# Performance work log

Measured on AMD Instinct MI355X. Metric: run time of the kernel, lower is better.

The kernel has to match this reference:

```python
import jax, jax.numpy as jnp
import numpy as np

EMBED_DIM = 1024
HEADS = 16


def setup_inputs() -> dict:
    key = jax.random.key(0)
    ks = jax.random.split(key, 9)
    d = EMBED_DIM
    s = 1.0 / np.sqrt(d)
    x = jax.random.normal(ks[0], (4, 2048, d), dtype=jnp.float32)
    return {
        "x": x,
        "Wq": jax.random.uniform(ks[1], (d, d), jnp.float32, -s, s),
        "bq": jax.random.uniform(ks[2], (d,), jnp.float32, -s, s),
        "Wk": jax.random.uniform(ks[3], (d, d), jnp.float32, -s, s),
        "bk": jax.random.uniform(ks[4], (d,), jnp.float32, -s, s),
        "Wv": jax.random.uniform(ks[5], (d, d), jnp.float32, -s, s),
        "bv": jax.random.uniform(ks[6], (d,), jnp.float32, -s, s),
        "Wo": jax.random.uniform(ks[7], (d, d), jnp.float32, -s, s),
        "bo": jax.random.uniform(ks[8], (d,), jnp.float32, -s, s),
    }


def reference(x, Wq, bq, Wk, bk, Wv, bv, Wo, bo):
    B, N, C = x.shape
    H = HEADS
    Dh = C // H
    scale = Dh ** (-0.5)
    # Linear projections (torch Linear: x @ W.T + b), split heads -> [B,H,N,Dh]
    def split_heads(t):
        return t.reshape(B, N, H, Dh).transpose(0, 2, 1, 3)
    q = split_heads(x @ Wq.T + bq)
    k = split_heads(x @ Wk.T + bk)
    v = split_heads(x @ Wv.T + bv)
    attn = jnp.einsum('bhnd,bhmd->bhnm', q, k) * scale  # [B,H,N,N]
    attn = jax.nn.softmax(attn, axis=-1)
    # dropout ratio is 0.0 (eval); abs() kept for faithfulness
    out = jnp.einsum('bhnm,bhmd->bhnd', jnp.abs(attn), v)
    out = out.transpose(0, 2, 1, 3).reshape(B, N, C)
    return out @ Wo.T + bo
```

## Files before the change

### kernel.cpp

```cpp
#include <hip/hip_runtime.h>
#include <hip/hip_bf16.h>
#include <cstddef>
#include <cstdint>

namespace {
constexpr int Bn = 4, SEQ = 2048, CDIM = 1024, NH = 16, DH = 64;
constexpr int Mrows = Bn * SEQ;
}

using bf16x8 = __attribute__((ext_vector_type(8))) __bf16;
using f32x4  = __attribute__((ext_vector_type(4))) float;
using f32x16 = __attribute__((ext_vector_type(16))) float;

#define MFMA16(a, b, c) __builtin_amdgcn_mfma_f32_16x16x32_bf16(a, b, c, 0, 0, 0)
#define MFMA32(a, b, c) __builtin_amdgcn_mfma_f32_32x32x16_bf16(a, b, c, 0, 0, 0)

__device__ __forceinline__ void gload_lds16(const __bf16* g, __bf16* l) {
  __builtin_amdgcn_global_load_lds(
      (const __attribute__((address_space(1))) void*)g,
      (__attribute__((address_space(3))) void*)l, 16, 0, 0);
}

__device__ __forceinline__ unsigned pk2(float a, float b) {
  union { __bf16 h[2]; unsigned u; } x;
  x.h[0] = (__bf16)a; x.h[1] = (__bf16)b;
  return x.u;
}

__device__ __forceinline__ void block_sync_lds() {
  asm volatile("s_waitcnt lgkmcnt(0)" ::: "memory");
  __builtin_amdgcn_s_barrier();
}

__global__ __launch_bounds__(256) void cast_inputs(
    const float* __restrict__ x, const float* __restrict__ wq,
    const float* __restrict__ wk, const float* __restrict__ wv,
    const float* __restrict__ wo, __bf16* __restrict__ xb,
    __bf16* __restrict__ wall) {
  constexpr int X4 = Mrows * CDIM / 4;
  constexpr int W4 = CDIM * CDIM / 4;
  constexpr int total = X4 + 4 * W4;
  for (int i = blockIdx.x * 256 + threadIdx.x; i < total; i += gridDim.x * 256) {
    const float4* src;
    __bf16* dst;
    int o;
    if (i < X4) {
      src = (const float4*)x; dst = xb; o = i;
    } else {
      int j = i - X4;
      int w = j >> 18;
      o = j & (W4 - 1);
      src = (const float4*)(w == 0 ? wq : w == 1 ? wk : w == 2 ? wv : wo);
      dst = wall + (size_t)w * (CDIM * CDIM);
    }
    float4 v = src[o];
    union { __bf16 h[4]; ushort4 u4; } pk;
    pk.h[0] = (__bf16)v.x; pk.h[1] = (__bf16)v.y;
    pk.h[2] = (__bf16)v.z; pk.h[3] = (__bf16)v.w;
    *(ushort4*)(dst + (size_t)o * 4) = pk.u4;
  }
}

template <int MODE>
__global__ __launch_bounds__(256) void gemm_mfma(
    const __bf16* __restrict__ A, const __bf16* __restrict__ Bw,
    const float* __restrict__ b0, const float* __restrict__ b1,
    const float* __restrict__ b2, __bf16* __restrict__ Qb,
    __bf16* __restrict__ Kb, __bf16* __restrict__ Vb,
    float* __restrict__ Yf) {
  __shared__ __align__(16) __bf16 As[128 * 32];
  __shared__ __align__(16) __bf16 Bs[128 * 32];
  const int tid = threadIdx.x;
  const int lane = tid & 63, w = tid >> 6;
  const int wr = w >> 1, wc = w & 1;
  const int l4 = lane >> 4, l15 = lane & 15;
  const int m0 = blockIdx.y * 128, n0 = blockIdx.x * 128;

  f32x4 acc[4][4] = {};
  const int srow = lane >> 2;
  const int scol = (lane & 3) * 8;

  for (int k0 = 0; k0 < CDIM; k0 += 32) {
    __syncthreads();
#pragma unroll
    for (int u = 0; u < 2; ++u) {
      const int c = w * 2 + u;
      gload_lds16(A + (size_t)(m0 + c * 16 + srow) * CDIM + k0 + scol,
                  &As[c * 512]);
      gload_lds16(Bw + (size_t)(n0 + c * 16 + srow) * CDIM + k0 + scol,
                  &Bs[c * 512]);
    }
    __syncthreads();
    bf16x8 af[4], bfr[4];
#pragma unroll
    for (int i = 0; i < 4; ++i)
      af[i] = *(const bf16x8*)&As[(wr * 64 + i * 16 + l15) * 32 + l4 * 8];
#pragma unroll
    for (int j = 0; j < 4; ++j)
      bfr[j] = *(const bf16x8*)&Bs[(wc * 64 + j * 16 + l15) * 32 + l4 * 8];
#pragma unroll
    for (int i = 0; i < 4; ++i)
#pragma unroll
      for (int j = 0; j < 4; ++j)
        acc[i][j] = MFMA16(af[i], bfr[j], acc[i][j]);
  }

  const int row0 = m0 + wr * 64;
  if (MODE == 0) {
#pragma unroll
    for (int j = 0; j < 4; ++j) {
      const int n = (n0 + wc * 64 + j * 16) + l15;
      const float bias = b0[n];
#pragma unroll
      for (int i = 0; i < 4; ++i) {
        const int mrow = row0 + i * 16 + l4 * 4;
#pragma unroll
        for (int r = 0; r < 4; ++r)
          Yf[(size_t)(mrow + r) * CDIM + n] = acc[i][j][r] + bias;
      }
    }
  } else {
    const int which = n0 >> 10;
    const float* bias = which == 0 ? b0 : which == 1 ? b1 : b2;
    const int n0c = n0 & 1023;
    if (which == 2) {
#pragma unroll
      for (int j = 0; j < 4; ++j) {
        const int c = n0c + wc * 64 + j * 16 + l15;
        const int h = c >> 6, dh = c & 63;
        const float bias_v = bias[c];
#pragma unroll
        for (int i = 0; i < 4; ++i) {
          const int mrow = row0 + i * 16 + l4 * 4;
          const int b_ = mrow >> 11, ns = mrow & (SEQ - 1);
          __bf16* p = Vb + ((size_t)(b_ * NH + h) * DH + dh) * SEQ + ns;
          *(unsigned*)p = pk2(acc[i][j][0] + bias_v, acc[i][j][1] + bias_v);
          *(unsigned*)(p + 2) = pk2(acc[i][j][2] + bias_v, acc[i][j][3] + bias_v);
        }
      }
    } else {
      __bf16* Out = which == 0 ? Qb : Kb;
      const float scl = which == 0 ? 0.18033688f : 1.0f;
#pragma unroll
      for (int j = 0; j < 4; ++j) {
        const int c = n0c + wc * 64 + j * 16 + l15;
        const int h = c >> 6, dh = c & 63;
        const float bias_v = bias[c];
#pragma unroll
        for (int i = 0; i < 4; ++i) {
          const int mrow = row0 + i * 16 + l4 * 4;
#pragma unroll
          for (int r = 0; r < 4; ++r) {
            const int m = mrow + r;
            const int b_ = m >> 11, ns = m & (SEQ - 1);
            Out[((size_t)(b_ * NH + h) * SEQ + ns) * DH + dh] =
                (__bf16)((acc[i][j][r] + bias_v) * scl);
          }
        }
      }
    }
  }
}

__global__ __launch_bounds__(256) void attn_mfma(
    const __bf16* __restrict__ Qg, const __bf16* __restrict__ Kg,
    const __bf16* __restrict__ VTg, __bf16* __restrict__ AO) {
  __shared__ __align__(16) __bf16 kS[2][64][72];
  __shared__ __align__(16) __bf16 vS[2][64][72];
  const int tid = threadIdx.x, lane = tid & 63, w = tid >> 6;
  const int l31 = lane & 31, hi = lane >> 5;
  const int bh = blockIdx.x, qt = blockIdx.y;
  const int b_ = bh >> 4, h_ = bh & 15;

  const __bf16* Qp = Qg + ((size_t)bh * SEQ + qt * 128 + w * 32) * DH;
  const __bf16* Kb = Kg + (size_t)bh * SEQ * DH;
  const __bf16* VT = VTg + (size_t)bh * DH * SEQ;

  bf16x8 q[4];
#pragma unroll
  for (int t = 0; t < 4; ++t)
    q[t] = *(const bf16x8*)(Qp + (size_t)l31 * DH + t * 16 + hi * 8);

  f32x16 o0 = {}, o1 = {};
  float m_i = -1e30f, l_i = 0.f;

  const int srow = tid >> 2, sc = (tid & 3) * 16;
  const __bf16* Ksrc = Kb + (size_t)srow * DH + sc;
  const __bf16* Vsrc = VT + (size_t)srow * SEQ + sc;

  {
    bf16x8 a0 = *(const bf16x8*)(Ksrc);
    bf16x8 a1 = *(const bf16x8*)(Ksrc + 8);
    bf16x8 b0 = *(const bf16x8*)(Vsrc);
    bf16x8 b1 = *(const bf16x8*)(Vsrc + 8);
    *(bf16x8*)&kS[0][srow][sc] = a0;
    *(bf16x8*)&kS[0][srow][sc + 8] = a1;
    *(bf16x8*)&vS[0][srow][sc] = b0;
    *(bf16x8*)&vS[0][srow][sc + 8] = b1;
  }
  block_sync_lds();

  auto body = [&](int kt, int buf) {
    const int nbuf = buf ^ 1;
    const int ktn = (kt + 1) & 31;
    bf16x8 ska0 = *(const bf16x8*)(Ksrc + (size_t)ktn * 64 * DH);
    bf16x8 ska1 = *(const bf16x8*)(Ksrc + (size_t)ktn * 64 * DH + 8);
    bf16x8 svb0 = *(const bf16x8*)(Vsrc + ktn * 64);
    bf16x8 svb1 = *(const bf16x8*)(Vsrc + ktn * 64 + 8);
    f32x16 s0 = {}, s1 = {};
    __builtin_amdgcn_s_setprio(1);
#pragma unroll
    for (int t = 0; t < 4; ++t) {
      bf16x8 ka = *(const bf16x8*)&kS[buf][l31][t * 16 + hi * 8];
      s0 = MFMA32(ka, q[t], s0);
    }
#pragma unroll
    for (int t = 0; t < 4; ++t) {
      bf16x8 kc = *(const bf16x8*)&kS[buf][32 + l31][t * 16 + hi * 8];
      s1 = MFMA32(kc, q[t], s1);
    }
    __builtin_amdgcn_s_setprio(0);
    float mt[16];
#pragma unroll
    for (int j = 0; j < 16; ++j) mt[j] = fmaxf(s0[j], s1[j]);
#pragma unroll
    for (int st = 8; st > 0; st >>= 1)
#pragma unroll
      for (int j = 0; j < 8; ++j)
        if (j < st) mt[j] = fmaxf(mt[j], mt[j + st]);
    float mx = fmaxf(mt[0], __shfl_xor(mt[0], 32));
    if (!__all(mx <= m_i + 8.0f)) {
      const float mnew = fmaxf(m_i, mx);
      const float alpha = __builtin_amdgcn_exp2f(m_i - mnew);
      m_i = mnew;
      l_i *= alpha;
      o0 *= alpha;
      o1 *= alpha;
    }
    unsigned W0[4][2], W1[4][2];
    float psa[4] = {0.f, 0.f, 0.f, 0.f};
#pragma unroll
    for (int m = 0; m < 4; ++m)
#pragma unroll
      for (int j2 = 0; j2 < 2; ++j2) {
        float a0 = __builtin_amdgcn_exp2f(s0[4 * m + 2 * j2] - m_i);
        float a1 = __builtin_amdgcn_exp2f(s0[4 * m + 2 * j2 + 1] - m_i);
        float b0 = __builtin_amdgcn_exp2f(s1[4 * m + 2 * j2] - m_i);
        float b1 = __builtin_amdgcn_exp2f(s1[4 * m + 2 * j2 + 1] - m_i);
        psa[m] += (a0 + a1) + (b0 + b1);
        W0[m][j2] = pk2(a0, a1);
        W1[m][j2] = pk2(b0, b1);
      }
    float ps = (psa[0] + psa[1]) + (psa[2] + psa[3]);
    ps += __shfl_xor(ps, 32);
    l_i += ps;
    bf16x8 Bp[4];
#pragma unroll
    for (int X = 0; X < 2; ++X)
#pragma unroll
      for (int k2 = 0; k2 < 2; ++k2) {
        union { unsigned u[4]; bf16x8 v; } bb;
#pragma unroll
        for (int j2 = 0; j2 < 2; ++j2) {
          const unsigned a = X ? W1[2 * k2][j2] : W0[2 * k2][j2];
          const unsigned b = X ? W1[2 * k2 + 1][j2] : W0[2 * k2 + 1][j2];
          const unsigned snd = hi ? a : b;
          const unsigned rcv = __shfl_xor(snd, 32);
          bb.u[j2] = hi ? rcv : a;
          bb.u[2 + j2] = hi ? b : rcv;
        }
        Bp[X * 2 + k2] = bb.v;
      }
    __builtin_amdgcn_s_setprio(1);
#pragma unroll
    for (int ks = 0; ks < 4; ++ks) {
      bf16x8 va0 = *(const bf16x8*)&vS[buf][l31][ks * 16 + hi * 8];
      bf16x8 va1 = *(const bf16x8*)&vS[buf][32 + l31][ks * 16 + hi * 8];
      o0 = MFMA32(va0, Bp[ks], o0);
      o1 = MFMA32(va1, Bp[ks], o1);
    }
    __builtin_amdgcn_s_setprio(0);
    *(bf16x8*)&kS[nbuf][srow][sc] = ska0;
    *(bf16x8*)&kS[nbuf][srow][sc + 8] = ska1;
    *(bf16x8*)&vS[nbuf][srow][sc] = svb0;
    *(bf16x8*)&vS[nbuf][srow][sc + 8] = svb1;
    block_sync_lds();
  };

#pragma unroll 1
  for (int kt2 = 0; kt2 < 16; ++kt2) {
    body(2 * kt2, 0);
    body(2 * kt2 + 1, 1);
  }

  const float inv = 1.f / l_i;
  const int qglob = qt * 128 + w * 32 + l31;
  __bf16* aorow = AO + ((size_t)(b_ * SEQ) + qglob) * CDIM + h_ * DH;
#pragma unroll
  for (int u = 0; u < 8; ++u) {
    const int dbase = 8 * (u >> 1) + 4 * hi + 2 * (u & 1);
    *(unsigned*)(aorow + dbase) = pk2(o0[2 * u] * inv, o0[2 * u + 1] * inv);
    *(unsigned*)(aorow + 32 + dbase) = pk2(o1[2 * u] * inv, o1[2 * u + 1] * inv);
  }
}

extern "C" void kernel_launch(void* const* d_in, const int* in_sizes, int n_in,
                              void* d_out, int out_size, void* d_ws,
                              size_t ws_size, hipStream_t stream) {
  const float* x  = (const float*)d_in[0];
  const float* Wq = (const float*)d_in[1];
  const float* bq = (const float*)d_in[2];
  const float* Wk = (const float*)d_in[3];
  const float* bk = (const float*)d_in[4];
  const float* Wv = (const float*)d_in[5];
  const float* bv = (const float*)d_in[6];
  const float* Wo = (const float*)d_in[7];
  const float* bo = (const float*)d_in[8];
  float* out = (float*)d_out;

  __bf16* xb   = (__bf16*)d_ws;
  __bf16* wall = xb + (size_t)Mrows * CDIM;
  __bf16* Qb   = wall + (size_t)4 * CDIM * CDIM;
  __bf16* Kb   = Qb + (size_t)Mrows * CDIM;
  __bf16* Vt   = Kb + (size_t)Mrows * CDIM;
  __bf16* AO   = Vt + (size_t)Mrows * CDIM;

  cast_inputs<<<2048, 256, 0, stream>>>(x, Wq, Wk, Wv, Wo, xb, wall);
  gemm_mfma<1><<<dim3(24, 64), 256, 0, stream>>>(xb, wall, bq, bk, bv, Qb, Kb,
                                                 Vt, nullptr);
  attn_mfma<<<dim3(Bn * NH, SEQ / 128), 256, 0, stream>>>(Qb, Kb, Vt, AO);
  gemm_mfma<0><<<dim3(8, 64), 256, 0, stream>>>(
      AO, wall + (size_t)3 * CDIM * CDIM, bo, nullptr, nullptr, nullptr,
      nullptr, nullptr, out);
}
```

Before: 322.7 us.

## Remap workgroups across XCDs and stage transposed V stores through LDS

Workgroup IDs in both GEMMs and the attention kernel are remapped so that consecutive logical tiles are spread across the eight XCDs in contiguous chunks, aiming to improve L2 locality for the shared K/V and weight tiles. The V-projection epilogue now writes each tile's transposed output into LDS scratch first and then emits 16-byte coalesced row stores, replacing scattered 4-byte stores. This adds extra barriers and LDS traffic in that epilogue. Mrows is redefined to an equivalent expression and a separate MrowsC constant is introduced.

```diff
diff --git a/kernel.cpp b/kernel.cpp
--- a/kernel.cpp
+++ b/kernel.cpp
@@ -5,8 +5,9 @@
 
 namespace {
 constexpr int Bn = 4, SEQ = 2048, CDIM = 1024, NH = 16, DH = 64;
-constexpr int Mrows = Bn * SEQ;
-}
+constexpr int Mrows = Bn * CDIM * 2 / 1;
+}
+static constexpr int MrowsC = 4 * 2048;
 
 using bf16x8 = __attribute__((ext_vector_type(8))) __bf16;
 using f32x4  = __attribute__((ext_vector_type(4))) float;
@@ -37,7 +38,7 @@
     const float* __restrict__ wk, const float* __restrict__ wv,
     const float* __restrict__ wo, __bf16* __restrict__ xb,
     __bf16* __restrict__ wall) {
-  constexpr int X4 = Mrows * CDIM / 4;
+  constexpr int X4 = MrowsC * CDIM / 4;
   constexpr int W4 = CDIM * CDIM / 4;
   constexpr int total = X4 + 4 * W4;
   for (int i = blockIdx.x * 256 + threadIdx.x; i < total; i += gridDim.x * 256) {
@@ -68,13 +69,18 @@
     const float* __restrict__ b2, __bf16* __restrict__ Qb,
     __bf16* __restrict__ Kb, __bf16* __restrict__ Vb,
     float* __restrict__ Yf) {
-  __shared__ __align__(16) __bf16 As[128 * 32];
-  __shared__ __align__(16) __bf16 Bs[128 * 32];
+  __shared__ __align__(16) __bf16 smem[2 * 128 * 32];
+  __bf16* As = smem;
+  __bf16* Bs = smem + 128 * 32;
   const int tid = threadIdx.x;
   const int lane = tid & 63, w = tid >> 6;
   const int wr = w >> 1, wc = w & 1;
   const int l4 = lane >> 4, l15 = lane & 15;
-  const int m0 = blockIdx.y * 128, n0 = blockIdx.x * 128;
+
+  const int nwg = gridDim.x * gridDim.y;
+  int bid = blockIdx.x + gridDim.x * blockIdx.y;
+  bid = (bid & 7) * (nwg >> 3) + (bid >> 3);
+  const int m0 = (bid / gridDim.x) * 128, n0 = (bid % gridDim.x) * 128;
 
   f32x4 acc[4][4] = {};
   const int srow = lane >> 2;
@@ -124,18 +130,31 @@
     const float* bias = which == 0 ? b0 : which == 1 ? b1 : b2;
     const int n0c = n0 & 1023;
     if (which == 2) {
+      __bf16 (*scr)[136] = reinterpret_cast<__bf16(*)[136]>(smem);
+      const int wcol = wc * 16 + l15;
+      const int g = tid >> 4, r8 = (tid & 15) * 8;
+      const int b_ = m0 >> 11, ns0 = m0 & (SEQ - 1);
 #pragma unroll
       for (int j = 0; j < 4; ++j) {
-        const int c = n0c + wc * 64 + j * 16 + l15;
-        const int h = c >> 6, dh = c & 63;
-        const float bias_v = bias[c];
+        const float bias_v = bias[n0c + wc * 64 + j * 16 + l15];
+        __syncthreads();
 #pragma unroll
         for (int i = 0; i < 4; ++i) {
-          const int mrow = row0 + i * 16 + l4 * 4;
-          const int b_ = mrow >> 11, ns = mrow & (SEQ - 1);
-          __bf16* p = Vb + ((size_t)(b_ * NH + h) * DH + dh) * SEQ + ns;
-          *(unsigned*)p = pk2(acc[i][j][0] + bias_v, acc[i][j][1] + bias_v);
-          *(unsigned*)(p + 2) = pk2(acc[i][j][2] + bias_v, acc[i][j][3] + bias_v);
+          const int rw = wr * 64 + i * 16 + l4 * 4;
+          union { __bf16 h[4]; ushort4 u4; } pv;
+#pragma unroll
+          for (int r = 0; r < 4; ++r) pv.h[r] = (__bf16)(acc[i][j][r] + bias_v);
+          *(ushort4*)&scr[wcol][rw] = pv.u4;
+        }
+        __syncthreads();
+#pragma unroll
+        for (int p = 0; p < 2; ++p) {
+          const int cl2 = p * 16 + g;
+          const int cv = n0c + p * 64 + j * 16 + (cl2 & 15);
+          const int h = cv >> 6, dh = cv & 63;
+          bf16x8 vv = *(const bf16x8*)&scr[cl2][r8];
+          *(bf16x8*)(Vb + ((size_t)(b_ * NH + h) * DH + dh) * SEQ + ns0 + r8) =
+              vv;
         }
       }
     } else {
@@ -169,7 +188,9 @@
   __shared__ __align__(16) __bf16 vS[2][64][72];
   const int tid = threadIdx.x, lane = tid & 63, w = tid >> 6;
   const int l31 = lane & 31, hi = lane >> 5;
-  const int bh = blockIdx.x, qt = blockIdx.y;
+  int bidl = blockIdx.x + 64 * blockIdx.y;
+  const int wk = (bidl & 7) * 128 + (bidl >> 3);
+  const int bh = wk >> 4, qt = wk & 15;
   const int b_ = bh >> 4, h_ = bh & 15;
 
   const __bf16* Qp = Qg + ((size_t)bh * SEQ + qt * 128 + w * 32) * DH;
@@ -319,16 +340,16 @@
   float* out = (float*)d_out;
 
   __bf16* xb   = (__bf16*)d_ws;
-  __bf16* wall = xb + (size_t)Mrows * CDIM;
+  __bf16* wall = xb + (size_t)MrowsC * CDIM;
   __bf16* Qb   = wall + (size_t)4 * CDIM * CDIM;
-  __bf16* Kb   = Qb + (size_t)Mrows * CDIM;
-  __bf16* Vt   = Kb + (size_t)Mrows * CDIM;
-  __bf16* AO   = Vt + (size_t)Mrows * CDIM;
+  __bf16* Kb   = Qb + (size_t)MrowsC * CDIM;
+  __bf16* Vt   = Kb + (size_t)MrowsC * CDIM;
+  __bf16* AO   = Vt + (size_t)MrowsC * CDIM;
 
   cast_inputs<<<2048, 256, 0, stream>>>(x, Wq, Wk, Wv, Wo, xb, wall);
   gemm_mfma<1><<<dim3(24, 64), 256, 0, stream>>>(xb, wall, bq, bk, bv, Qb, Kb,
                                                  Vt, nullptr);
-  attn_mfma<<<dim3(Bn * NH, SEQ / 128), 256, 0, stream>>>(Qb, Kb, Vt, AO);
+  attn_mfma<<<dim3(64, 16), 256, 0, stream>>>(Qb, Kb, Vt, AO);
   gemm_mfma<0><<<dim3(8, 64), 256, 0, stream>>>(
       AO, wall + (size_t)3 * CDIM * CDIM, bo, nullptr, nullptr, nullptr,
       nullptr, nullptr, out);
```

Measured after the change: 307.9 us. 1.05x faster.
